# Kernel tuning notes

Measured on AMD Instinct MI355X. Metric: run time of the kernel, lower is better.

Reference implementation:

```python
import jax, jax.numpy as jnp
import numpy as np

N_EMBD = 2048
N_HEAD = 32
HEAD_SIZE = 64          # n_embd // n_head
MIX_DIM = 64            # RWKV-6 time-mix LoRA dim
DECAY_DIM = 128         # RWKV-6 decay LoRA dim
BATCH = 1024
STATE_ROWS = (2 + HEAD_SIZE) * 1  # single block, i = 0


def setup_inputs() -> dict:
    key = jax.random.key(0)
    ks = jax.random.split(key, 32)
    rn = lambda k, shp, s=0.02: jax.random.normal(k, shp, jnp.float32) * s
    d = {}
    d['x'] = jax.random.normal(ks[0], (BATCH, N_EMBD), jnp.float32)
    d['state'] = jax.random.normal(ks[1], (BATCH, STATE_ROWS, N_EMBD), jnp.float32) * 0.1
    d['ln1_w'] = jnp.ones((N_EMBD,), jnp.float32)
    d['ln1_b'] = jnp.zeros((N_EMBD,), jnp.float32)
    d['ln2_w'] = jnp.ones((N_EMBD,), jnp.float32)
    d['ln2_b'] = jnp.zeros((N_EMBD,), jnp.float32)
    d['maa_x'] = rn(ks[2], (N_EMBD,), 0.1)
    d['maa_w'] = rn(ks[3], (N_EMBD,), 0.1)
    d['maa_k'] = rn(ks[4], (N_EMBD,), 0.1)
    d['maa_v'] = rn(ks[5], (N_EMBD,), 0.1)
    d['maa_r'] = rn(ks[6], (N_EMBD,), 0.1)
    d['maa_g'] = rn(ks[7], (N_EMBD,), 0.1)
    d['maa_w1'] = rn(ks[8], (N_EMBD, 5 * MIX_DIM))
    d['maa_w2'] = rn(ks[9], (5, MIX_DIM, N_EMBD))
    d['decay'] = rn(ks[10], (N_EMBD,), 0.5) - 4.0  # typical negative log-decay
    d['decay_w1'] = rn(ks[11], (N_EMBD, DECAY_DIM))
    d['decay_w2'] = rn(ks[12], (DECAY_DIM, N_EMBD))
    d['faaaa'] = rn(ks[13], (N_HEAD, HEAD_SIZE, 1), 0.1)
    d['Wr'] = rn(ks[14], (N_EMBD, N_EMBD))
    d['Wk'] = rn(ks[15], (N_EMBD, N_EMBD))
    d['Wv'] = rn(ks[16], (N_EMBD, N_EMBD))
    d['Wo'] = rn(ks[17], (N_EMBD, N_EMBD))
    d['Wg'] = rn(ks[18], (N_EMBD, N_EMBD))
    d['gn_w'] = jnp.ones((N_EMBD,), jnp.float32)
    d['gn_b'] = jnp.zeros((N_EMBD,), jnp.float32)
    d['ffn_maa_k'] = rn(ks[19], (N_EMBD,), 0.1)
    d['ffn_maa_r'] = rn(ks[20], (N_EMBD,), 0.1)
    d['ffn_Wk'] = rn(ks[21], (N_EMBD, N_EMBD))
    d['ffn_Wr'] = rn(ks[22], (N_EMBD, N_EMBD))
    d['ffn_Wv'] = rn(ks[23], (N_EMBD, N_EMBD))
    d['i'] = 0
    return d


def _ln(x, w, b):
    mu = jnp.mean(x, -1, keepdims=True)
    var = jnp.var(x, -1, keepdims=True)
    return (x - mu) * jax.lax.rsqrt(var + 1e-5) * w + b


def reference(x, state, ln1_w, ln1_b, ln2_w, ln2_b,
              maa_x, maa_w, maa_k, maa_v, maa_r, maa_g, maa_w1, maa_w2,
              decay, decay_w1, decay_w2, faaaa,
              Wr, Wk, Wv, Wo, Wg, gn_w, gn_b,
              ffn_maa_k, ffn_maa_r, ffn_Wk, ffn_Wr, ffn_Wv, i):
    B = x.shape[0]
    H, S = N_HEAD, HEAD_SIZE
    # ---------------- time mixing ----------------
    xn = _ln(x, ln1_w, ln1_b)
    i1 = (2 + S) * i + 1
    sx = state[:, i1] - xn                                  # token shift delta
    xxx = xn + sx * maa_x
    xxx = jnp.tanh(xxx @ maa_w1).reshape(B, 5, 1, MIX_DIM)
    xxx = jnp.matmul(xxx, maa_w2).reshape(B, 5, N_EMBD)     # [B,5,E]
    mw, mk, mv, mr, mg = (xxx[:, j] for j in range(5))
    xw = xn + sx * (maa_w + mw)
    xk = xn + sx * (maa_k + mk)
    xv = xn + sx * (maa_v + mv)
    xr = xn + sx * (maa_r + mr)
    xg = xn + sx * (maa_g + mg)
    w = decay + jnp.tanh(xw @ decay_w1) @ decay_w2          # [B,E]
    w = jnp.exp(-jnp.exp(w.reshape(B, H, S, 1)))            # decay gate
    r = (xr @ Wr.T).reshape(B, H, 1, S)
    k = (xk @ Wk.T).reshape(B, H, S, 1)
    v = (xv @ Wv.T).reshape(B, H, 1, S)
    g = jax.nn.silu(xg @ Wg.T)
    s = state[:, (2 + S) * i + 2:(2 + S) * (i + 1), :].reshape(B, H, S, S)
    a = jnp.matmul(k, v)                                    # [B,H,S,S] outer product
    y = jnp.matmul(r, faaaa * a + s).reshape(B, N_EMBD)     # wkv readout
    # group norm (n_head groups over n_embd channels)
    yg = y.reshape(B, H, S)
    mu = jnp.mean(yg, -1, keepdims=True)
    var = jnp.var(yg, -1, keepdims=True)
    yg = ((yg - mu) * jax.lax.rsqrt(var + 1e-5)).reshape(B, N_EMBD) * gn_w + gn_b
    x1 = x + (yg * g) @ Wo.T
    # ---------------- channel mixing ----------------
    xn2 = _ln(x1, ln2_w, ln2_b)
    i0 = (2 + S) * i
    sx2 = state[:, i0] - xn2
    xk2 = xn2 + sx2 * ffn_maa_k
    xr2 = xn2 + sx2 * ffn_maa_r
    rr = jax.nn.sigmoid(xr2 @ ffn_Wr.T)
    kk = jnp.square(jax.nn.relu(xk2 @ ffn_Wk.T))
    return x1 + rr * (kk @ ffn_Wv.T)
```

## Files before the change

kernel.cpp:

```cpp
#include <hip/hip_runtime.h>
#include <cstdint>
#include <cstddef>

typedef unsigned short u16;
typedef __attribute__((ext_vector_type(8))) short bf16x8;
typedef __attribute__((ext_vector_type(4))) float f32x4;

#define DEV __device__ __forceinline__

DEV u16 f2bf(float f) {
  uint32_t b = __float_as_uint(f);
  b += 0x7fffu + ((b >> 16) & 1u);
  return (u16)(b >> 16);
}
DEV float bf2f(u16 u) { return __uint_as_float(((uint32_t)u) << 16); }

DEV void gl16(const u16* g, u16* l) {
  __builtin_amdgcn_global_load_lds(
      (const __attribute__((address_space(1))) void*)g,
      (__attribute__((address_space(3))) void*)l, 16, 0, 0);
}

struct CvtArgs { const float* s[8]; };

__global__ __launch_bounds__(256) void k_cvt(CvtArgs a,
                                             const float* __restrict__ w1,
                                             const float* __restrict__ w2,
                                             u16* __restrict__ dst,
                                             u16* __restrict__ w1t,
                                             u16* __restrict__ w2t) {
  if (blockIdx.x < 16384) {
    size_t idx = ((size_t)blockIdx.x * 256 + threadIdx.x) * 8;
    int w = (int)(idx >> 22);
    size_t off = idx & ((1u << 22) - 1);
    const float* s = a.s[w];
    float4 v0 = *(const float4*)(s + off);
    float4 v1 = *(const float4*)(s + off + 4);
    uint4 p; u16* pl = (u16*)&p;
    pl[0] = f2bf(v0.x); pl[1] = f2bf(v0.y); pl[2] = f2bf(v0.z); pl[3] = f2bf(v0.w);
    pl[4] = f2bf(v1.x); pl[5] = f2bf(v1.y); pl[6] = f2bf(v1.z); pl[7] = f2bf(v1.w);
    *(uint4*)(dst + ((size_t)w << 22) + off) = p;
  } else {
    int idx = (blockIdx.x - 16384) * 256 + threadIdx.x;
    if (idx < 655360) {
      int n = idx >> 11, k = idx & 2047;
      w1t[idx] = f2bf(w1[(size_t)k * 320 + n]);
    } else {
      int r = idx - 655360;
      int j = r >> 17, q = r & 131071;
      int n = q >> 6, k2 = q & 63;
      w2t[r] = f2bf(w2[((size_t)(j + 1) * 64 + k2) * 2048 + n]);
    }
  }
}

__global__ __launch_bounds__(256) void k_tanhpack(const float* __restrict__ p2,
                                                  u16* __restrict__ xb) {
  int idx = blockIdx.x * 256 + threadIdx.x;
  float s = p2[idx] + p2[327680 + idx] + p2[2 * 327680 + idx] + p2[3 * 327680 + idx];
  xb[idx] = f2bf(tanhf(s));
}

__global__ __launch_bounds__(256) void k_act(const u16* __restrict__ p8,
                                             u16* __restrict__ rr, u16* __restrict__ kk) {
  const size_t S = 2097152;
  int gid = blockIdx.x * 256 + threadIdx.x;
  size_t e0 = (size_t)(gid & 262143) * 8;
  int isk = gid >= 262144;
  const u16* base = p8 + (isk ? 4 * S : 0) + e0;
  float acc[8] = {};
#pragma unroll
  for (int s = 0; s < 4; ++s) {
    uint4 v = *(const uint4*)(base + (size_t)s * S);
    u16* vl = (u16*)&v;
#pragma unroll
    for (int j = 0; j < 8; ++j) acc[j] += bf2f(vl[j]);
  }
  uint4 p; u16* pl = (u16*)&p;
  if (!isk) {
#pragma unroll
    for (int j = 0; j < 8; ++j) pl[j] = f2bf(1.f / (1.f + __expf(-acc[j])));
    *(uint4*)(rr + e0) = p;
  } else {
#pragma unroll
    for (int j = 0; j < 8; ++j) { float r = acc[j] > 0.f ? acc[j] : 0.f; pl[j] = f2bf(r * r); }
    *(uint4*)(kk + e0) = p;
  }
}

__global__ __launch_bounds__(256) void k_fin(const float* __restrict__ x1,
                                             const u16* __restrict__ p9,
                                             const u16* __restrict__ rr,
                                             float* __restrict__ out) {
  const size_t S = 2097152;
  size_t e0 = ((size_t)blockIdx.x * 256 + threadIdx.x) * 8;
  float acc[8] = {};
#pragma unroll
  for (int s = 0; s < 4; ++s) {
    uint4 v = *(const uint4*)(p9 + (size_t)s * S + e0);
    u16* vl = (u16*)&v;
#pragma unroll
    for (int j = 0; j < 8; ++j) acc[j] += bf2f(vl[j]);
  }
  float4 x0 = *(const float4*)(x1 + e0), x4 = *(const float4*)(x1 + e0 + 4);
  float xv[8] = {x0.x, x0.y, x0.z, x0.w, x4.x, x4.y, x4.z, x4.w};
  uint4 rv = *(const uint4*)(rr + e0); u16* rl = (u16*)&rv;
  float o[8];
#pragma unroll
  for (int j = 0; j < 8; ++j) o[j] = xv[j] + bf2f(rl[j]) * acc[j];
  *(float4*)(out + e0) = make_float4(o[0], o[1], o[2], o[3]);
  *(float4*)(out + e0 + 4) = make_float4(o[4], o[5], o[6], o[7]);
}

__global__ __launch_bounds__(256) void k_ln_mix1(
    const float* __restrict__ x, const float* __restrict__ state,
    const int* __restrict__ ip,
    const float* __restrict__ lw, const float* __restrict__ lb,
    const float* __restrict__ mx,
    u16* __restrict__ xn_o, u16* __restrict__ sx_o, u16* __restrict__ a1_o) {
  int b = blockIdx.x, t = threadIdx.x;
  const float* xr = x + (size_t)b * 2048;
  float4 v0 = *(const float4*)(xr + t * 8);
  float4 v1 = *(const float4*)(xr + t * 8 + 4);
  float xv[8] = {v0.x, v0.y, v0.z, v0.w, v1.x, v1.y, v1.z, v1.w};
  float s1 = 0.f, s2 = 0.f;
#pragma unroll
  for (int j = 0; j < 8; ++j) { s1 += xv[j]; s2 += xv[j] * xv[j]; }
#pragma unroll
  for (int off = 32; off; off >>= 1) { s1 += __shfl_xor(s1, off); s2 += __shfl_xor(s2, off); }
  __shared__ float ls1[4], ls2[4];
  int w = t >> 6;
  if ((t & 63) == 0) { ls1[w] = s1; ls2[w] = s2; }
  __syncthreads();
  s1 = ls1[0] + ls1[1] + ls1[2] + ls1[3];
  s2 = ls2[0] + ls2[1] + ls2[2] + ls2[3];
  float mu = s1 * (1.0f / 2048.0f);
  float var = s2 * (1.0f / 2048.0f) - mu * mu;
  float rs = rsqrtf(var + 1e-5f);
  const float* st = state + ((size_t)b * 66 + (size_t)66 * ip[0] + 1) * 2048;
  int e0 = t * 8;
  uint4 xnp, sxp, a1p;
  u16* xnl = (u16*)&xnp; u16* sxl = (u16*)&sxp; u16* a1l = (u16*)&a1p;
#pragma unroll
  for (int j = 0; j < 8; ++j) {
    int e = e0 + j;
    float xn = (xv[j] - mu) * rs * lw[e] + lb[e];
    float sxv = st[e] - xn;
    xnl[j] = f2bf(xn); sxl[j] = f2bf(sxv); a1l[j] = f2bf(xn + sxv * mx[e]);
  }
  size_t o = (size_t)b * 2048 + e0;
  *(uint4*)(xn_o + o) = xnp;
  *(uint4*)(sx_o + o) = sxp;
  *(uint4*)(a1_o + o) = a1p;
}

__global__ __launch_bounds__(256) void k_ln_mix2(
    const float* __restrict__ x, const u16* __restrict__ p6,
    const float* __restrict__ state, const int* __restrict__ ip,
    const float* __restrict__ lw, const float* __restrict__ lb,
    const float* __restrict__ mk, const float* __restrict__ mr,
    u16* __restrict__ xk_o, u16* __restrict__ xr_o, float* __restrict__ x1_o) {
  const size_t S = 2097152;
  int b = blockIdx.x, t = threadIdx.x;
  size_t off = (size_t)b * 2048 + t * 8;
  float4 v0 = *(const float4*)(x + off);
  float4 v1 = *(const float4*)(x + off + 4);
  float xv[8] = {v0.x, v0.y, v0.z, v0.w, v1.x, v1.y, v1.z, v1.w};
#pragma unroll
  for (int s = 0; s < 4; ++s) {
    uint4 v = *(const uint4*)(p6 + (size_t)s * S + off);
    u16* vl = (u16*)&v;
#pragma unroll
    for (int j = 0; j < 8; ++j) xv[j] += bf2f(vl[j]);
  }
  *(float4*)(x1_o + off) = make_float4(xv[0], xv[1], xv[2], xv[3]);
  *(float4*)(x1_o + off + 4) = make_float4(xv[4], xv[5], xv[6], xv[7]);
  float s1 = 0.f, s2 = 0.f;
#pragma unroll
  for (int j = 0; j < 8; ++j) { s1 += xv[j]; s2 += xv[j] * xv[j]; }
#pragma unroll
  for (int off2 = 32; off2; off2 >>= 1) { s1 += __shfl_xor(s1, off2); s2 += __shfl_xor(s2, off2); }
  __shared__ float ls1[4], ls2[4];
  int w = t >> 6;
  if ((t & 63) == 0) { ls1[w] = s1; ls2[w] = s2; }
  __syncthreads();
  s1 = ls1[0] + ls1[1] + ls1[2] + ls1[3];
  s2 = ls2[0] + ls2[1] + ls2[2] + ls2[3];
  float mu = s1 * (1.0f / 2048.0f);
  float var = s2 * (1.0f / 2048.0f) - mu * mu;
  float rs = rsqrtf(var + 1e-5f);
  const float* st = state + ((size_t)b * 66 + (size_t)66 * ip[0] + 0) * 2048;
  int e0 = t * 8;
  uint4 xkp, xrp;
  u16* xkl = (u16*)&xkp; u16* xrl = (u16*)&xrp;
#pragma unroll
  for (int j = 0; j < 8; ++j) {
    int e = e0 + j;
    float xn = (xv[j] - mu) * rs * lw[e] + lb[e];
    float sxv = st[e] - xn;
    xkl[j] = f2bf(xn + sxv * mk[e]);
    xrl[j] = f2bf(xn + sxv * mr[e]);
  }
  *(uint4*)(xk_o + off) = xkp;
  *(uint4*)(xr_o + off) = xrp;
}

enum { EP_STORE = 0, EP_SILU, EP_MIX, EP_STOREF };

struct GemmDesc {
  const u16* A; const u16* B; void* C;
  const void* p1; const void* p2; const float* pvec;
  int lda, ldb, ldc, N, K, k0, ep;
};
struct GemmBatch { GemmDesc g[8]; int bpg; };

__global__ __launch_bounds__(256, 3) void k_gemm(GemmBatch bat) {
  int gi = blockIdx.x / bat.bpg;
  int bid = blockIdx.x % bat.bpg;
  GemmDesc g = bat.g[gi];
  int ntn = (g.N + 127) >> 7;
  int m0 = (bid / ntn) << 7;
  int n0 = (bid % ntn) << 7;
  __shared__ u16 As[2][128 * 32];
  __shared__ u16 Bs[2][128 * 32];
  int t = threadIdx.x, w = t >> 6, lane = t & 63;
  int wm = w >> 1, wn = w & 1;
  int lr = lane & 15, kb = (lane >> 4) * 8;
  const u16* Ab = g.A + (size_t)(m0 + w * 32 + (lane >> 2)) * g.lda + (lane & 3) * 8;
  const u16* Bb = g.B + (size_t)(n0 + w * 32 + (lane >> 2)) * g.ldb + (lane & 3) * 8;
  int a16 = 16 * g.lda, b16 = 16 * g.ldb;
  int aoff = (w * 32) * 32;
  f32x4 acc[4][4] = {};
  int nt = g.K >> 5;

  auto stage = [&](int buf, int kk) {
    u16* Ad = (u16*)As + buf * 4096 + aoff;
    u16* Bd = (u16*)Bs + buf * 4096 + aoff;
    gl16(Ab + kk, Ad);
    gl16(Ab + kk + a16, Ad + 512);
    gl16(Bb + kk, Bd);
    gl16(Bb + kk + b16, Bd + 512);
  };

  stage(0, g.k0);
  __syncthreads();
  int cur = 0;
  for (int ti = 0; ti < nt; ++ti) {
    if (ti + 1 < nt) stage(cur ^ 1, g.k0 + (ti + 1) * 32);
    const u16* Ac = (const u16*)As + cur * 4096;
// ... 11 lines not shown
      for (int n = 0; n < 4; ++n)
        acc[m][n] = __builtin_amdgcn_mfma_f32_16x16x32_bf16(af[m], bfr[n], acc[m][n], 0, 0, 0);
    __syncthreads();
    cur ^= 1;
  }

  int ep = g.ep;
#pragma unroll
  for (int m = 0; m < 4; ++m) {
    int grow0 = m0 + wm * 64 + m * 16 + (lane >> 4) * 4;
#pragma unroll
    for (int n = 0; n < 4; ++n) {
      int gc = n0 + wn * 64 + n * 16 + lr;
      if (gc >= g.N) continue;
#pragma unroll
      for (int q = 0; q < 4; ++q) {
        size_t ci = (size_t)(grow0 + q) * g.ldc + gc;
        float v = acc[m][n][q];
        switch (ep) {
          case EP_STORE: ((u16*)g.C)[ci] = f2bf(v); break;
          case EP_MIX: {
            float xn = bf2f(((const u16*)g.p1)[ci]);
            float sxv = bf2f(((const u16*)g.p2)[ci]);
            ((u16*)g.C)[ci] = f2bf(xn + sxv * (g.pvec[gc] + v));
          } break;
          case EP_STOREF: ((float*)g.C)[ci] = v; break;
          default: break;
        }
      }
    }
  }
}

__global__ __launch_bounds__(512, 2) void k_gemm2(GemmBatch bat) {
  extern __shared__ u16 lds[];
  int nwg = gridDim.x;
  int wg0 = blockIdx.x;
  int wg = (wg0 & 7) * (nwg >> 3) + (wg0 >> 3);
  int gi = wg / bat.bpg;
  int bid = wg % bat.bpg;
  GemmDesc g = bat.g[gi];
  int ntn = (g.N + 255) >> 8;
  int m0 = (bid / ntn) << 7;
  int n0 = (bid % ntn) << 8;
  int t = threadIdx.x, wv = t >> 6, lane = t & 63;
  int wm = wv >> 2, wn = wv & 3;
  int lr = lane & 15, hi = lane >> 4;

  const u16* asrc[2]; const u16* bsrc[4];
#pragma unroll
  for (int j = 0; j < 2; ++j) {
    int cid = t + 512 * j, r = cid >> 3, c = cid & 7;
    asrc[j] = g.A + (size_t)(m0 + r) * g.lda + ((c ^ (r & 7)) << 3);
  }
#pragma unroll
  for (int j = 0; j < 4; ++j) {
    int cid = t + 512 * j, r = cid >> 3, c = cid & 7;
    bsrc[j] = g.B + (size_t)(n0 + r) * g.ldb + ((c ^ (r & 7)) << 3);
  }
  int au = wv * 512;

  auto stage = [&](int buf, int k) {
    u16* base = lds + buf * 24576;
#pragma unroll
    for (int j = 0; j < 2; ++j) gl16(asrc[j] + k, base + au + j * 4096);
#pragma unroll
    for (int j = 0; j < 4; ++j) gl16(bsrc[j] + k, base + 8192 + au + j * 4096);
  };

  int arow[4], brow[4];
#pragma unroll
  for (int m = 0; m < 4; ++m) arow[m] = wm * 64 + m * 16 + lr;
#pragma unroll
  for (int n = 0; n < 4; ++n) brow[n] = wn * 64 + n * 16 + lr;

  f32x4 acc[4][4] = {};
  int nt = g.K >> 6;
  stage(0, g.k0);
  if (nt > 1) stage(1, g.k0 + 64);

  for (int ti = 0; ti < nt; ++ti) {
    if (ti + 1 < nt) asm volatile("s_waitcnt vmcnt(6)" ::: "memory");
    else             asm volatile("s_waitcnt vmcnt(0)" ::: "memory");
    __builtin_amdgcn_sched_barrier(0);
    __builtin_amdgcn_s_barrier();
    __builtin_amdgcn_sched_barrier(0);
    const u16* buf = lds + (ti % 3) * 24576;
    bf16x8 af[4][2], bf[4][2];
#pragma unroll
    for (int m = 0; m < 4; ++m)
#pragma unroll
      for (int ks = 0; ks < 2; ++ks)
        af[m][ks] = *(const bf16x8*)(buf + arow[m] * 64 + ((((ks << 2) + hi) ^ (arow[m] & 7)) << 3));
#pragma unroll
    for (int n = 0; n < 4; ++n)
#pragma unroll
      for (int ks = 0; ks < 2; ++ks)
        bf[n][ks] = *(const bf16x8*)(buf + 8192 + brow[n] * 64 + ((((ks << 2) + hi) ^ (brow[n] & 7)) << 3));
    if (ti + 2 < nt) stage((ti + 2) % 3, g.k0 + (ti + 2) * 64);
    __builtin_amdgcn_s_setprio(1);
#pragma unroll
    for (int m = 0; m < 4; ++m)
#pragma unroll
      for (int n = 0; n < 4; ++n)
#pragma unroll
        for (int ks = 0; ks < 2; ++ks)
          acc[m][n] = __builtin_amdgcn_mfma_f32_16x16x32_bf16(af[m][ks], bf[n][ks], acc[m][n], 0, 0, 0);
    __builtin_amdgcn_s_setprio(0);
  }

  int ep = g.ep;
#pragma unroll
  for (int m = 0; m < 4; ++m) {
    int grow0 = m0 + wm * 64 + m * 16 + hi * 4;
#pragma unroll
    for (int n = 0; n < 4; ++n) {
      int gc = n0 + wn * 64 + n * 16 + lr;
#pragma unroll
      for (int q = 0; q < 4; ++q) {
        size_t ci = (size_t)(grow0 + q) * g.ldc + gc;
        float v = acc[m][n][q];
        switch (ep) {
          case EP_STORE: ((u16*)g.C)[ci] = f2bf(v); break;
          case EP_SILU:  ((u16*)g.C)[ci] = f2bf(v / (1.f + __expf(-v))); break;
          case EP_STOREF: ((float*)g.C)[ci] = v; break;
          default: break;
        }
      }
    }
  }
}

__global__ __launch_bounds__(512, 2) void k_gemm3(GemmBatch bat) {
  extern __shared__ u16 lds[];
  int nwg = gridDim.x;
  int wg0 = blockIdx.x;
  int wg = (wg0 & 7) * (nwg >> 3) + (wg0 >> 3);
  GemmDesc g = bat.g[wg / bat.bpg];
  int bid = wg % bat.bpg;
  int ntn = g.N >> 8;
  int m0 = (bid / ntn) << 8;
  int n0 = (bid % ntn) << 8;
  int t = threadIdx.x, wv = t >> 6, lane = t & 63;
  int wm = wv >> 2, wn = wv & 3;
  int lr = lane & 15, hi = lane >> 4;

  const u16* asrc[4]; const u16* bsrc[4];
#pragma unroll
  for (int j = 0; j < 4; ++j) {
    int cid = t + 512 * j, r = cid >> 3, c = cid & 7;
    asrc[j] = g.A + (size_t)(m0 + r) * g.lda + ((c ^ (r & 7)) << 3);
    bsrc[j] = g.B + (size_t)(n0 + r) * g.ldb + ((c ^ (r & 7)) << 3);
  }
  int au = wv * 512;

  auto stage = [&](int buf, int k) {
    u16* ab = lds + buf * 32768 + au;
    u16* bb = lds + buf * 32768 + 16384 + au;
#pragma unroll
    for (int j = 0; j < 4; ++j) gl16(asrc[j] + k, ab + j * 4096);
#pragma unroll
    for (int j = 0; j < 4; ++j) gl16(bsrc[j] + k, bb + j * 4096);
  };

  int arow[8], brow[4];
#pragma unroll
  for (int m = 0; m < 8; ++m) arow[m] = wm * 128 + m * 16 + lr;
#pragma unroll
  for (int n = 0; n < 4; ++n) brow[n] = wn * 64 + n * 16 + lr;

  f32x4 acc[8][4] = {};
  int nt = g.K >> 6;
  stage(0, g.k0);
  if (nt > 1) stage(1, g.k0 + 64);

  for (int ti = 0; ti < nt; ++ti) {
    if (ti + 1 < nt) asm volatile("s_waitcnt vmcnt(8)" ::: "memory");
    else             asm volatile("s_waitcnt vmcnt(0)" ::: "memory");
    __builtin_amdgcn_sched_barrier(0);
    __builtin_amdgcn_s_barrier();
    __builtin_amdgcn_sched_barrier(0);
    const u16* buf = lds + (ti & 1) * 32768;
#pragma unroll
    for (int ks = 0; ks < 2; ++ks) {
      bf16x8 af[8], bf[4];
#pragma unroll
      for (int m = 0; m < 8; ++m)
        af[m] = *(const bf16x8*)(buf + arow[m] * 64 + ((((ks << 2) + hi) ^ (arow[m] & 7)) << 3));
#pragma unroll
      for (int n = 0; n < 4; ++n)
        bf[n] = *(const bf16x8*)(buf + 16384 + brow[n] * 64 + ((((ks << 2) + hi) ^ (brow[n] & 7)) << 3));
      __builtin_amdgcn_s_setprio(1);
#pragma unroll
      for (int m = 0; m < 8; ++m)
#pragma unroll
        for (int n = 0; n < 4; ++n)
          acc[m][n] = __builtin_amdgcn_mfma_f32_16x16x32_bf16(af[m], bf[n], acc[m][n], 0, 0, 0);
      __builtin_amdgcn_s_setprio(0);
    }
    __builtin_amdgcn_sched_barrier(0);
    __builtin_amdgcn_s_barrier();
    __builtin_amdgcn_sched_barrier(0);
    if (ti + 2 < nt) stage(ti & 1, g.k0 + (ti + 2) * 64);
  }

#pragma unroll
  for (int m = 0; m < 8; ++m) {
    int grow0 = m0 + wm * 128 + m * 16 + hi * 4;
#pragma unroll
    for (int n = 0; n < 4; ++n) {
      int gc = n0 + wn * 64 + n * 16 + lr;
#pragma unroll
      for (int q = 0; q < 4; ++q)
        ((u16*)g.C)[(size_t)(grow0 + q) * g.ldc + gc] = f2bf(acc[m][n][q]);
    }
  }
}

__global__ __launch_bounds__(256) void k_wkv(
    const u16* __restrict__ p4,
    const float* __restrict__ state, const int* __restrict__ ip,
    const float* __restrict__ fa, const float* __restrict__ gw,
    const float* __restrict__ gbias, u16* __restrict__ t_o) {
  const size_t S = 2097152;
  int t = threadIdx.x, w = t >> 6, lane = t & 63;
  int flat = blockIdx.x * 4 + w;
  int b = flat >> 5, h = flat & 31;
  size_t base = ((size_t)b << 11) + (h << 6) + lane;
  float r  = bf2f(p4[base])         + bf2f(p4[S + base]);
  float kv = bf2f(p4[2 * S + base]) + bf2f(p4[3 * S + base]);
  float vv = bf2f(p4[4 * S + base]) + bf2f(p4[5 * S + base]);
  float gs = bf2f(p4[6 * S + base]) + bf2f(p4[7 * S + base]);
  float gg = gs / (1.f + __expf(-gs));
  float f  = fa[(h << 6) + lane];
  __shared__ float rs[4][64];
  rs[w][lane] = r;
  __syncthreads();
  float c = r * f * kv;
#pragma unroll
  for (int off = 32; off; off >>= 1) c += __shfl_xor(c, off);

  const float* sp = state + ((size_t)b * 66 + (size_t)66 * ip[0] + 2 + 2 * h) * 2048;
  int q = lane >> 4, jj = lane & 15;
  float yp0 = 0.f, yp1 = 0.f, yp2 = 0.f, yp3 = 0.f;
#pragma unroll
  for (int ib = 0; ib < 16; ++ib) {
    int i = ib * 4 + q;
// ... 40 lines not shown
  const float* faaaa  = (const float*)d_in[17];
  const float* Wr     = (const float*)d_in[18];
  const float* Wk     = (const float*)d_in[19];
  const float* Wv     = (const float*)d_in[20];
  const float* Wo     = (const float*)d_in[21];
  const float* Wg     = (const float*)d_in[22];
  const float* gn_w   = (const float*)d_in[23];
  const float* gn_b   = (const float*)d_in[24];
  const float* fmk    = (const float*)d_in[25];
  const float* fmr    = (const float*)d_in[26];
  const float* fWk    = (const float*)d_in[27];
  const float* fWr    = (const float*)d_in[28];
  const float* fWv    = (const float*)d_in[29];
  const int*   ip     = (const int*)d_in[30];
  float* out = (float*)d_out;

  char* wsb = (char*)d_ws;
  const size_t MB = 1ull << 20;
  u16* wbf   = (u16*)(wsb + 0 * MB);
  u16* w1t   = (u16*)(wsb + 64 * MB);
  u16* w2t   = (u16*)(wsb + 66 * MB);
  u16* xn    = (u16*)(wsb + 68 * MB);
  u16* sx    = (u16*)(wsb + 72 * MB);
  u16* a1    = (u16*)(wsb + 76 * MB);
  float* p2  = (float*)(wsb + 80 * MB);
  u16* xxx   = (u16*)(wsb + 86 * MB);
  u16* xk    = (u16*)(wsb + 87 * MB);
  u16* xv    = (u16*)(wsb + 91 * MB);
  u16* xr    = (u16*)(wsb + 95 * MB);
  u16* xg    = (u16*)(wsb + 99 * MB);
  u16* p4    = (u16*)(wsb + 103 * MB);
  u16* tb    = (u16*)(wsb + 135 * MB);
  u16* p6    = (u16*)(wsb + 139 * MB);
  float* x1  = (float*)(wsb + 155 * MB);
  u16* xk2   = (u16*)(wsb + 163 * MB);
  u16* xr2   = (u16*)(wsb + 167 * MB);
  u16* p8    = (u16*)(wsb + 171 * MB);
  u16* rr    = (u16*)(wsb + 203 * MB);
  u16* kkb   = (u16*)(wsb + 207 * MB);
  u16* p9    = (u16*)(wsb + 211 * MB);

  const size_t WSQ = 4194304, S = 2097152;
  u16* bWr = wbf + 0 * WSQ; u16* bWk = wbf + 1 * WSQ; u16* bWv = wbf + 2 * WSQ;
  u16* bWg = wbf + 3 * WSQ; u16* bWo = wbf + 4 * WSQ; u16* bfWr = wbf + 5 * WSQ;
  u16* bfWk = wbf + 6 * WSQ; u16* bfWv = wbf + 7 * WSQ;

  auto mkd = [](const u16* A, const u16* B, void* C, const void* p1,
                const void* p2_, const float* pvec, int lda, int ldb, int ldc,
                int N, int K, int k0, int epf) {
    GemmDesc d; d.A = A; d.B = B; d.C = C; d.p1 = p1; d.p2 = p2_; d.pvec = pvec;
    d.lda = lda; d.ldb = ldb; d.ldc = ldc; d.N = N; d.K = K; d.k0 = k0; d.ep = epf;
    return d;
  };

  static const int LDS2 = 147456;
  static const int LDS3 = 131072;
  hipFuncSetAttribute((const void*)k_gemm2,
                      hipFuncAttributeMaxDynamicSharedMemorySize, LDS2);
  hipFuncSetAttribute((const void*)k_gemm3,
                      hipFuncAttributeMaxDynamicSharedMemorySize, LDS3);

  {
    CvtArgs ca; ca.s[0] = Wr; ca.s[1] = Wk; ca.s[2] = Wv; ca.s[3] = Wg;
    ca.s[4] = Wo; ca.s[5] = fWr; ca.s[6] = fWk; ca.s[7] = fWv;
    k_cvt<<<20992, 256, 0, stream>>>(ca, maa_w1, maa_w2, wbf, w1t, w2t);
  }

  k_ln_mix1<<<1024, 256, 0, stream>>>(x, state, ip, ln1_w, ln1_b, maa_x, xn, sx, a1);

  {
    GemmBatch g{}; g.bpg = 8 * 3;
    for (int j = 0; j < 4; ++j)
      g.g[j] = mkd(a1, w1t, p2 + (size_t)j * 327680, nullptr, nullptr, nullptr,
                   2048, 2048, 320, 320, 512, j * 512, EP_STOREF);
    k_gemm<<<96, 256, 0, stream>>>(g);
  }
  k_tanhpack<<<1280, 256, 0, stream>>>(p2, xxx);

  {
    GemmBatch g{}; g.bpg = 8 * 16;
    const float* mv[4] = {maa_k, maa_v, maa_r, maa_g};
    u16* tv[4] = {xk, xv, xr, xg};
    for (int j = 1; j <= 4; ++j)
      g.g[j - 1] = mkd(xxx + j * 64, w2t + (size_t)(j - 1) * 131072, tv[j - 1],
                       xn, sx, mv[j - 1], 320, 64, 2048, 2048, 64, 0, EP_MIX);
    k_gemm<<<512, 256, 0, stream>>>(g);
  }

  {
    GemmBatch g{}; g.bpg = 32;
    const u16* av[4] = {xr, xk, xv, xg};
    const u16* bv[4] = {bWr, bWk, bWv, bWg};
    for (int q = 0; q < 4; ++q)
      for (int s = 0; s < 2; ++s)
        g.g[q * 2 + s] = mkd(av[q], bv[q], p4 + (size_t)(q * 2 + s) * S,
                             nullptr, nullptr, nullptr, 2048, 2048, 2048,
                             2048, 1024, s * 1024, EP_STORE);
    k_gemm3<<<256, 512, LDS3, stream>>>(g);
  }

  k_wkv<<<8192, 256, 0, stream>>>(p4, state, ip, faaaa, gn_w, gn_b, tb);

  {
    GemmBatch g{}; g.bpg = 8 * 8;
    for (int s = 0; s < 4; ++s)
      g.g[s] = mkd(tb, bWo, p6 + (size_t)s * S, nullptr, nullptr, nullptr,
                   2048, 2048, 2048, 2048, 512, s * 512, EP_STORE);
    k_gemm2<<<256, 512, LDS2, stream>>>(g);
  }

  k_ln_mix2<<<1024, 256, 0, stream>>>(x, p6, state, ip, ln2_w, ln2_b, fmk, fmr,
                                      xk2, xr2, x1);

  {
    GemmBatch g{}; g.bpg = 32;
    for (int s = 0; s < 4; ++s) {
      g.g[s]     = mkd(xr2, bfWr, p8 + (size_t)s * S, nullptr, nullptr, nullptr,
                       2048, 2048, 2048, 2048, 512, s * 512, EP_STORE);
      g.g[4 + s] = mkd(xk2, bfWk, p8 + (size_t)(4 + s) * S, nullptr, nullptr, nullptr,
                       2048, 2048, 2048, 2048, 512, s * 512, EP_STORE);
    }
    k_gemm3<<<256, 512, LDS3, stream>>>(g);
  }
  k_act<<<2048, 256, 0, stream>>>(p8, rr, kkb);

  {
    GemmBatch g{}; g.bpg = 8 * 8;
    for (int s = 0; s < 4; ++s)
      g.g[s] = mkd(kkb, bfWv, p9 + (size_t)s * S, nullptr, nullptr, nullptr,
                   2048, 2048, 2048, 2048, 512, s * 512, EP_STORE);
    k_gemm2<<<256, 512, LDS2, stream>>>(g);
  }

  k_fin<<<1024, 256, 0, stream>>>(x1, p9, rr, out);
}
```

Measured before the change: 326.3 us.

## Rework gemm3 with 4-stage k32 pipeline, drop gemm2, fuse LN1 into convert

New measurement: 349.2 us. +7.0%, slower.

```diff
diff --git a/kernel.cpp b/kernel.cpp
--- a/kernel.cpp
+++ b/kernel.cpp
@@ -23,12 +23,15 @@
 
 struct CvtArgs { const float* s[8]; };
 
-__global__ __launch_bounds__(256) void k_cvt(CvtArgs a,
-                                             const float* __restrict__ w1,
-                                             const float* __restrict__ w2,
-                                             u16* __restrict__ dst,
-                                             u16* __restrict__ w1t,
-                                             u16* __restrict__ w2t) {
+__global__ __launch_bounds__(256) void k_cvt_ln(
+    CvtArgs a, const float* __restrict__ w1, const float* __restrict__ w2,
+    u16* __restrict__ dst, u16* __restrict__ w1t, u16* __restrict__ w2t,
+    const float* __restrict__ x, const float* __restrict__ state,
+    const int* __restrict__ ip,
+    const float* __restrict__ lw, const float* __restrict__ lb,
+    const float* __restrict__ mx,
+    u16* __restrict__ xn_o, u16* __restrict__ sx_o, u16* __restrict__ a1_o) {
+  __shared__ float ls1[4], ls2[4];
   if (blockIdx.x < 16384) {
     size_t idx = ((size_t)blockIdx.x * 256 + threadIdx.x) * 8;
     int w = (int)(idx >> 22);
@@ -40,7 +43,7 @@
     pl[0] = f2bf(v0.x); pl[1] = f2bf(v0.y); pl[2] = f2bf(v0.z); pl[3] = f2bf(v0.w);
     pl[4] = f2bf(v1.x); pl[5] = f2bf(v1.y); pl[6] = f2bf(v1.z); pl[7] = f2bf(v1.w);
     *(uint4*)(dst + ((size_t)w << 22) + off) = p;
-  } else {
+  } else if (blockIdx.x < 20992) {
     int idx = (blockIdx.x - 16384) * 256 + threadIdx.x;
     if (idx < 655360) {
       int n = idx >> 11, k = idx & 2047;
@@ -51,6 +54,40 @@
       int n = q >> 6, k2 = q & 63;
       w2t[r] = f2bf(w2[((size_t)(j + 1) * 64 + k2) * 2048 + n]);
     }
+  } else {
+    int b = blockIdx.x - 20992, t = threadIdx.x;
+    const float* xr = x + (size_t)b * 2048;
+    float4 v0 = *(const float4*)(xr + t * 8);
+    float4 v1 = *(const float4*)(xr + t * 8 + 4);
+    float xv[8] = {v0.x, v0.y, v0.z, v0.w, v1.x, v1.y, v1.z, v1.w};
+    float s1 = 0.f, s2 = 0.f;
+#pragma unroll
+    for (int j = 0; j < 8; ++j) { s1 += xv[j]; s2 += xv[j] * xv[j]; }
+#pragma unroll
+    for (int off = 32; off; off >>= 1) { s1 += __shfl_xor(s1, off); s2 += __shfl_xor(s2, off); }
+    int w = t >> 6;
+    if ((t & 63) == 0) { ls1[w] = s1; ls2[w] = s2; }
+    __syncthreads();
+    s1 = ls1[0] + ls1[1] + ls1[2] + ls1[3];
+    s2 = ls2[0] + ls2[1] + ls2[2] + ls2[3];
+    float mu = s1 * (1.0f / 2048.0f);
+    float var = s2 * (1.0f / 2048.0f) - mu * mu;
+    float rs = rsqrtf(var + 1e-5f);
+    const float* st = state + ((size_t)b * 66 + (size_t)66 * ip[0] + 1) * 2048;
+    int e0 = t * 8;
+    uint4 xnp, sxp, a1p;
+    u16* xnl = (u16*)&xnp; u16* sxl = (u16*)&sxp; u16* a1l = (u16*)&a1p;
+#pragma unroll
+    for (int j = 0; j < 8; ++j) {
+      int e = e0 + j;
+      float xn = (xv[j] - mu) * rs * lw[e] + lb[e];
+      float sxv = st[e] - xn;
+      xnl[j] = f2bf(xn); sxl[j] = f2bf(sxv); a1l[j] = f2bf(xn + sxv * mx[e]);
+    }
+    size_t o = (size_t)b * 2048 + e0;
+    *(uint4*)(xn_o + o) = xnp;
+    *(uint4*)(sx_o + o) = sxp;
+    *(uint4*)(a1_o + o) = a1p;
   }
 }
 
@@ -96,7 +133,7 @@
   size_t e0 = ((size_t)blockIdx.x * 256 + threadIdx.x) * 8;
   float acc[8] = {};
 #pragma unroll
-  for (int s = 0; s < 4; ++s) {
+  for (int s = 0; s < 8; ++s) {
     uint4 v = *(const uint4*)(p9 + (size_t)s * S + e0);
     u16* vl = (u16*)&v;
 #pragma unroll
@@ -110,48 +147,6 @@
   for (int j = 0; j < 8; ++j) o[j] = xv[j] + bf2f(rl[j]) * acc[j];
   *(float4*)(out + e0) = make_float4(o[0], o[1], o[2], o[3]);
   *(float4*)(out + e0 + 4) = make_float4(o[4], o[5], o[6], o[7]);
-}
-
-__global__ __launch_bounds__(256) void k_ln_mix1(
-    const float* __restrict__ x, const float* __restrict__ state,
-    const int* __restrict__ ip,
-    const float* __restrict__ lw, const float* __restrict__ lb,
-    const float* __restrict__ mx,
-    u16* __restrict__ xn_o, u16* __restrict__ sx_o, u16* __restrict__ a1_o) {
-  int b = blockIdx.x, t = threadIdx.x;
-  const float* xr = x + (size_t)b * 2048;
-  float4 v0 = *(const float4*)(xr + t * 8);
-  float4 v1 = *(const float4*)(xr + t * 8 + 4);
-  float xv[8] = {v0.x, v0.y, v0.z, v0.w, v1.x, v1.y, v1.z, v1.w};
-  float s1 = 0.f, s2 = 0.f;
-#pragma unroll
-  for (int j = 0; j < 8; ++j) { s1 += xv[j]; s2 += xv[j] * xv[j]; }
-#pragma unroll
-  for (int off = 32; off; off >>= 1) { s1 += __shfl_xor(s1, off); s2 += __shfl_xor(s2, off); }
-  __shared__ float ls1[4], ls2[4];
-  int w = t >> 6;
-  if ((t & 63) == 0) { ls1[w] = s1; ls2[w] = s2; }
-  __syncthreads();
-  s1 = ls1[0] + ls1[1] + ls1[2] + ls1[3];
-  s2 = ls2[0] + ls2[1] + ls2[2] + ls2[3];
-  float mu = s1 * (1.0f / 2048.0f);
-  float var = s2 * (1.0f / 2048.0f) - mu * mu;
-  float rs = rsqrtf(var + 1e-5f);
-  const float* st = state + ((size_t)b * 66 + (size_t)66 * ip[0] + 1) * 2048;
-  int e0 = t * 8;
-  uint4 xnp, sxp, a1p;
-  u16* xnl = (u16*)&xnp; u16* sxl = (u16*)&sxp; u16* a1l = (u16*)&a1p;
-#pragma unroll
-  for (int j = 0; j < 8; ++j) {
-    int e = e0 + j;
-    float xn = (xv[j] - mu) * rs * lw[e] + lb[e];
-    float sxv = st[e] - xn;
-    xnl[j] = f2bf(xn); sxl[j] = f2bf(sxv); a1l[j] = f2bf(xn + sxv * mx[e]);
-  }
-  size_t o = (size_t)b * 2048 + e0;
-  *(uint4*)(xn_o + o) = xnp;
-  *(uint4*)(sx_o + o) = sxp;
-  *(uint4*)(a1_o + o) = a1p;
 }
 
 __global__ __launch_bounds__(256) void k_ln_mix2(
@@ -167,7 +162,7 @@
   float4 v1 = *(const float4*)(x + off + 4);
   float xv[8] = {v0.x, v0.y, v0.z, v0.w, v1.x, v1.y, v1.z, v1.w};
 #pragma unroll
-  for (int s = 0; s < 4; ++s) {
+  for (int s = 0; s < 8; ++s) {
     uint4 v = *(const uint4*)(p6 + (size_t)s * S + off);
     u16* vl = (u16*)&v;
 #pragma unroll
@@ -292,105 +287,6 @@
   }
 }
 
-__global__ __launch_bounds__(512, 2) void k_gemm2(GemmBatch bat) {
-  extern __shared__ u16 lds[];
-  int nwg = gridDim.x;
-  int wg0 = blockIdx.x;
-  int wg = (wg0 & 7) * (nwg >> 3) + (wg0 >> 3);
-  int gi = wg / bat.bpg;
-  int bid = wg % bat.bpg;
-  GemmDesc g = bat.g[gi];
-  int ntn = (g.N + 255) >> 8;
-  int m0 = (bid / ntn) << 7;
-  int n0 = (bid % ntn) << 8;
-  int t = threadIdx.x, wv = t >> 6, lane = t & 63;
-  int wm = wv >> 2, wn = wv & 3;
-  int lr = lane & 15, hi = lane >> 4;
-
-  const u16* asrc[2]; const u16* bsrc[4];
-#pragma unroll
-  for (int j = 0; j < 2; ++j) {
-    int cid = t + 512 * j, r = cid >> 3, c = cid & 7;
-    asrc[j] = g.A + (size_t)(m0 + r) * g.lda + ((c ^ (r & 7)) << 3);
-  }
-#pragma unroll
-  for (int j = 0; j < 4; ++j) {
-    int cid = t + 512 * j, r = cid >> 3, c = cid & 7;
-    bsrc[j] = g.B + (size_t)(n0 + r) * g.ldb + ((c ^ (r & 7)) << 3);
-  }
-  int au = wv * 512;
-
-  auto stage = [&](int buf, int k) {
-    u16* base = lds + buf * 24576;
-#pragma unroll
-    for (int j = 0; j < 2; ++j) gl16(asrc[j] + k, base + au + j * 4096);
-#pragma unroll
-    for (int j = 0; j < 4; ++j) gl16(bsrc[j] + k, base + 8192 + au + j * 4096);
-  };
-
-  int arow[4], brow[4];
-#pragma unroll
-  for (int m = 0; m < 4; ++m) arow[m] = wm * 64 + m * 16 + lr;
-#pragma unroll
-  for (int n = 0; n < 4; ++n) brow[n] = wn * 64 + n * 16 + lr;
-
-  f32x4 acc[4][4] = {};
-  int nt = g.K >> 6;
-  stage(0, g.k0);
-  if (nt > 1) stage(1, g.k0 + 64);
-
-  for (int ti = 0; ti < nt; ++ti) {
-    if (ti + 1 < nt) asm volatile("s_waitcnt vmcnt(6)" ::: "memory");
-    else             asm volatile("s_waitcnt vmcnt(0)" ::: "memory");
-    __builtin_amdgcn_sched_barrier(0);
-    __builtin_amdgcn_s_barrier();
-    __builtin_amdgcn_sched_barrier(0);
-    const u16* buf = lds + (ti % 3) * 24576;
-    bf16x8 af[4][2], bf[4][2];
-#pragma unroll
-    for (int m = 0; m < 4; ++m)
-#pragma unroll
-      for (int ks = 0; ks < 2; ++ks)
-        af[m][ks] = *(const bf16x8*)(buf + arow[m] * 64 + ((((ks << 2) + hi) ^ (arow[m] & 7)) << 3));
-#pragma unroll
-    for (int n = 0; n < 4; ++n)
-#pragma unroll
-      for (int ks = 0; ks < 2; ++ks)
-        bf[n][ks] = *(const bf16x8*)(buf + 8192 + brow[n] * 64 + ((((ks << 2) + hi) ^ (brow[n] & 7)) << 3));
-    if (ti + 2 < nt) stage((ti + 2) % 3, g.k0 + (ti + 2) * 64);
-    __builtin_amdgcn_s_setprio(1);
-#pragma unroll
-    for (int m = 0; m < 4; ++m)
-#pragma unroll
-      for (int n = 0; n < 4; ++n)
-#pragma unroll
-        for (int ks = 0; ks < 2; ++ks)
-          acc[m][n] = __builtin_amdgcn_mfma_f32_16x16x32_bf16(af[m][ks], bf[n][ks], acc[m][n], 0, 0, 0);
-    __builtin_amdgcn_s_setprio(0);
-  }
-
-  int ep = g.ep;
-#pragma unroll
-  for (int m = 0; m < 4; ++m) {
-    int grow0 = m0 + wm * 64 + m * 16 + hi * 4;
-#pragma unroll
-    for (int n = 0; n < 4; ++n) {
-      int gc = n0 + wn * 64 + n * 16 + lr;
-#pragma unroll
-      for (int q = 0; q < 4; ++q) {
-        size_t ci = (size_t)(grow0 + q) * g.ldc + gc;
-        float v = acc[m][n][q];
-        switch (ep) {
-          case EP_STORE: ((u16*)g.C)[ci] = f2bf(v); break;
-          case EP_SILU:  ((u16*)g.C)[ci] = f2bf(v / (1.f + __expf(-v))); break;
-          case EP_STOREF: ((float*)g.C)[ci] = v; break;
-          default: break;
-        }
-      }
-    }
-  }
-}
-
 __global__ __launch_bounds__(512, 2) void k_gemm3(GemmBatch bat) {
   extern __shared__ u16 lds[];
   int nwg = gridDim.x;
@@ -405,65 +301,85 @@
   int wm = wv >> 2, wn = wv & 3;
   int lr = lane & 15, hi = lane >> 4;
 
-  const u16* asrc[4]; const u16* bsrc[4];
-#pragma unroll
-  for (int j = 0; j < 4; ++j) {
-    int cid = t + 512 * j, r = cid >> 3, c = cid & 7;
-    asrc[j] = g.A + (size_t)(m0 + r) * g.lda + ((c ^ (r & 7)) << 3);
-    bsrc[j] = g.B + (size_t)(n0 + r) * g.ldb + ((c ^ (r & 7)) << 3);
-  }
+  int r = t >> 2;
+  int cc = (((t & 3) ^ (r & 3)) << 3);
+  const u16* sa0 = g.A + (size_t)(m0 + r) * g.lda + cc;
+  const u16* sa1 = g.A + (size_t)(m0 + 128 + r) * g.lda + cc;
+  const u16* sb0 = g.B + (size_t)(n0 + r) * g.ldb + cc;
+  const u16* sb1 = g.B + (size_t)(n0 + 128 + r) * g.ldb + cc;
   int au = wv * 512;
-
-  auto stage = [&](int buf, int k) {
-    u16* ab = lds + buf * 32768 + au;
-    u16* bb = lds + buf * 32768 + 16384 + au;
-#pragma unroll
-    for (int j = 0; j < 4; ++j) gl16(asrc[j] + k, ab + j * 4096);
-#pragma unroll
-    for (int j = 0; j < 4; ++j) gl16(bsrc[j] + k, bb + j * 4096);
-  };
-
-  int arow[8], brow[4];
-#pragma unroll
-  for (int m = 0; m < 8; ++m) arow[m] = wm * 128 + m * 16 + lr;
-#pragma unroll
-  for (int n = 0; n < 4; ++n) brow[n] = wn * 64 + n * 16 + lr;
+  u16* dummy = lds + 65536 + au;
+
+  int aswz = (hi ^ (lr & 3)) << 3;
+  int abase = wm * 4096 + lr * 32 + aswz;
+  int bbase = 8192 + (wv & 2) * 2048 + (wv & 1) * 2048 + lr * 32 + aswz;
+
+  int nt = g.K >> 5;
+  {
+    int k0e = g.k0;
+    gl16(sa0 + k0e, lds + au);            gl16(sb0 + k0e, lds + 8192 + au);
+    gl16(sa1 + k0e, lds + 4096 + au);     gl16(sb1 + k0e, lds + 12288 + au);
+    int k1e = g.k0 + 32;
+    gl16(sa0 + k1e, lds + 16384 + au);    gl16(sb0 + k1e, lds + 16384 + 8192 + au);
+    gl16(sa1 + k1e, lds + 16384 + 4096 + au); gl16(sb1 + k1e, lds + 16384 + 12288 + au);
+  }
+  asm volatile("s_waitcnt vmcnt(4)" ::: "memory");
+  __builtin_amdgcn_sched_barrier(0);
+  __builtin_amdgcn_s_barrier();
+  __builtin_amdgcn_sched_barrier(0);
 
   f32x4 acc[8][4] = {};
-  int nt = g.K >> 6;
-  stage(0, g.k0);
-  if (nt > 1) stage(1, g.k0 + 64);
-
-  for (int ti = 0; ti < nt; ++ti) {
-    if (ti + 1 < nt) asm volatile("s_waitcnt vmcnt(8)" ::: "memory");
-    else             asm volatile("s_waitcnt vmcnt(0)" ::: "memory");
+  for (int kt = 0; kt < nt; ++kt) {
+    const u16* bp = lds + (kt & 3) * 16384;
+    int real = (kt + 2 < nt);
+    int tgt = real ? kt + 2 : nt - 1;
+    int ko = g.k0 + tgt * 32;
+    u16* db = real ? lds + ((kt + 2) & 3) * 16384 : (u16*)0;
+
+    gl16(sa0 + ko, real ? db + au : dummy);
+    gl16(sb0 + ko, real ? db + 8192 + au : dummy);
+    bf16x8 a0_[8], bA[2];
+#pragma unroll
+    for (int m = 0; m < 8; ++m) a0_[m] = *(const bf16x8*)(bp + abase + m * 512);
+    bA[0] = *(const bf16x8*)(bp + bbase);
+    bA[1] = *(const bf16x8*)(bp + bbase + 512);
+    asm volatile("s_waitcnt vmcnt(4)" ::: "memory");
     __builtin_amdgcn_sched_barrier(0);
     __builtin_amdgcn_s_barrier();
     __builtin_amdgcn_sched_barrier(0);
-    const u16* buf = lds + (ti & 1) * 32768;
-#pragma unroll
-    for (int ks = 0; ks < 2; ++ks) {
-      bf16x8 af[8], bf[4];
-#pragma unroll
-      for (int m = 0; m < 8; ++m)
-        af[m] = *(const bf16x8*)(buf + arow[m] * 64 + ((((ks << 2) + hi) ^ (arow[m] & 7)) << 3));
-#pragma unroll
-      for (int n = 0; n < 4; ++n)
-        bf[n] = *(const bf16x8*)(buf + 16384 + brow[n] * 64 + ((((ks << 2) + hi) ^ (brow[n] & 7)) << 3));
-      __builtin_amdgcn_s_setprio(1);
-#pragma unroll
-      for (int m = 0; m < 8; ++m)
-#pragma unroll
-        for (int n = 0; n < 4; ++n)
-          acc[m][n] = __builtin_amdgcn_mfma_f32_16x16x32_bf16(af[m], bf[n], acc[m][n], 0, 0, 0);
-      __builtin_amdgcn_s_setprio(0);
-    }
+    __builtin_amdgcn_s_setprio(1);
+#pragma unroll
+    for (int m = 0; m < 8; ++m) {
+      acc[m][0] = __builtin_amdgcn_mfma_f32_16x16x32_bf16(a0_[m], bA[0], acc[m][0], 0, 0, 0);
+      acc[m][1] = __builtin_amdgcn_mfma_f32_16x16x32_bf16(a0_[m], bA[1], acc[m][1], 0, 0, 0);
+    }
+    __builtin_amdgcn_s_setprio(0);
     __builtin_amdgcn_sched_barrier(0);
     __builtin_amdgcn_s_barrier();
     __builtin_amdgcn_sched_barrier(0);
-    if (ti + 2 < nt) stage(ti & 1, g.k0 + (ti + 2) * 64);
-  }
-
+
+    gl16(sa1 + ko, real ? db + 4096 + au : dummy);
+    gl16(sb1 + ko, real ? db + 12288 + au : dummy);
+    bf16x8 bB[2];
+    bB[0] = *(const bf16x8*)(bp + bbase + 1024);
+    bB[1] = *(const bf16x8*)(bp + bbase + 1536);
+    asm volatile("s_waitcnt vmcnt(4)" ::: "memory");
+    __builtin_amdgcn_sched_barrier(0);
+    __builtin_amdgcn_s_barrier();
+    __builtin_amdgcn_sched_barrier(0);
+    __builtin_amdgcn_s_setprio(1);
+#pragma unroll
+    for (int m = 0; m < 8; ++m) {
+      acc[m][2] = __builtin_amdgcn_mfma_f32_16x16x32_bf16(a0_[m], bB[0], acc[m][2], 0, 0, 0);
+      acc[m][3] = __builtin_amdgcn_mfma_f32_16x16x32_bf16(a0_[m], bB[1], acc[m][3], 0, 0, 0);
+    }
+    __builtin_amdgcn_s_setprio(0);
+    __builtin_amdgcn_sched_barrier(0);
+    __builtin_amdgcn_s_barrier();
+    __builtin_amdgcn_sched_barrier(0);
+  }
+
+  int ep = g.ep;
 #pragma unroll
   for (int m = 0; m < 8; ++m) {
     int grow0 = m0 + wm * 128 + m * 16 + hi * 4;
@@ -471,8 +387,12 @@
     for (int n = 0; n < 4; ++n) {
       int gc = n0 + wn * 64 + n * 16 + lr;
 #pragma unroll
-      for (int q = 0; q < 4; ++q)
-        ((u16*)g.C)[(size_t)(grow0 + q) * g.ldc + gc] = f2bf(acc[m][n][q]);
+      for (int q = 0; q < 4; ++q) {
+        size_t ci = (size_t)(grow0 + q) * g.ldc + gc;
+        float v = acc[m][n][q];
+        if (ep == EP_STOREF) ((float*)g.C)[ci] = v;
+        else                 ((u16*)g.C)[ci] = f2bf(v);
+      }
     }
   }
 }
@@ -579,13 +499,13 @@
   u16* p4    = (u16*)(wsb + 103 * MB);
   u16* tb    = (u16*)(wsb + 135 * MB);
   u16* p6    = (u16*)(wsb + 139 * MB);
-  float* x1  = (float*)(wsb + 155 * MB);
-  u16* xk2   = (u16*)(wsb + 163 * MB);
-  u16* xr2   = (u16*)(wsb + 167 * MB);
-  u16* p8    = (u16*)(wsb + 171 * MB);
-  u16* rr    = (u16*)(wsb + 203 * MB);
-  u16* kkb   = (u16*)(wsb + 207 * MB);
-  u16* p9    = (u16*)(wsb + 211 * MB);
+  float* x1  = (float*)(wsb + 171 * MB);
+  u16* xk2   = (u16*)(wsb + 179 * MB);
+  u16* xr2   = (u16*)(wsb + 183 * MB);
+  u16* p8    = (u16*)(wsb + 187 * MB);
+  u16* rr    = (u16*)(wsb + 219 * MB);
+  u16* kkb   = (u16*)(wsb + 223 * MB);
+  u16* p9    = (u16*)(wsb + 227 * MB);
 
   const size_t WSQ = 4194304, S = 2097152;
   u16* bWr = wbf + 0 * WSQ; u16* bWk = wbf + 1 * WSQ; u16* bWv = wbf + 2 * WSQ;
@@ -600,20 +520,16 @@
     return d;
   };
 
-  static const int LDS2 = 147456;
-  static const int LDS3 = 131072;
-  hipFuncSetAttribute((const void*)k_gemm2,
-                      hipFuncAttributeMaxDynamicSharedMemorySize, LDS2);
+  static const int LDS3 = 139264;
   hipFuncSetAttribute((const void*)k_gemm3,
                       hipFuncAttributeMaxDynamicSharedMemorySize, LDS3);
 
   {
     CvtArgs ca; ca.s[0] = Wr; ca.s[1] = Wk; ca.s[2] = Wv; ca.s[3] = Wg;
     ca.s[4] = Wo; ca.s[5] = fWr; ca.s[6] = fWk; ca.s[7] = fWv;
-    k_cvt<<<20992, 256, 0, stream>>>(ca, maa_w1, maa_w2, wbf, w1t, w2t);
-  }
-
-  k_ln_mix1<<<1024, 256, 0, stream>>>(x, state, ip, ln1_w, ln1_b, maa_x, xn, sx, a1);
+    k_cvt_ln<<<22016, 256, 0, stream>>>(ca, maa_w1, maa_w2, wbf, w1t, w2t,
+                                        x, state, ip, ln1_w, ln1_b, maa_x, xn, sx, a1);
+  }
 
   {
     GemmBatch g{}; g.bpg = 8 * 3;
@@ -649,11 +565,11 @@
   k_wkv<<<8192, 256, 0, stream>>>(p4, state, ip, faaaa, gn_w, gn_b, tb);
 
   {
-    GemmBatch g{}; g.bpg = 8 * 8;
-    for (int s = 0; s < 4; ++s)
+    GemmBatch g{}; g.bpg = 32;
+    for (int s = 0; s < 8; ++s)
       g.g[s] = mkd(tb, bWo, p6 + (size_t)s * S, nullptr, nullptr, nullptr,
-                   2048, 2048, 2048, 2048, 512, s * 512, EP_STORE);
-    k_gemm2<<<256, 512, LDS2, stream>>>(g);
+                   2048, 2048, 2048, 2048, 256, s * 256, EP_STORE);
+    k_gemm3<<<256, 512, LDS3, stream>>>(g);
   }
 
   k_ln_mix2<<<1024, 256, 0, stream>>>(x, p6, state, ip, ln2_w, ln2_b, fmk, fmr,
@@ -672,11 +588,11 @@
   k_act<<<2048, 256, 0, stream>>>(p8, rr, kkb);
 
   {
-    GemmBatch g{}; g.bpg = 8 * 8;
-    for (int s = 0; s < 4; ++s)
+    GemmBatch g{}; g.bpg = 32;
+    for (int s = 0; s < 8; ++s)
       g.g[s] = mkd(kkb, bfWv, p9 + (size_t)s * S, nullptr, nullptr, nullptr,
-                   2048, 2048, 2048, 2048, 512, s * 512, EP_STORE);
-    k_gemm2<<<256, 512, LDS2, stream>>>(g);
+                   2048, 2048, 2048, 2048, 256, s * 256, EP_STORE);
+    k_gemm3<<<256, 512, LDS3, stream>>>(g);
   }
 
   k_fin<<<1024, 256, 0, stream>>>(x1, p9, rr, out);
```

## Overlap big weight bf16 conversion with small LoRA GEMMs and fuse LN into cvt

Applied to the files above, without the earlier changes.

Measured after the change: 320.2 us. Within noise of the previous version (-1.9%).

```diff
diff --git a/kernel.cpp b/kernel.cpp
--- a/kernel.cpp
+++ b/kernel.cpp
@@ -23,25 +23,17 @@
 
 struct CvtArgs { const float* s[8]; };
 
-__global__ __launch_bounds__(256) void k_cvt(CvtArgs a,
-                                             const float* __restrict__ w1,
-                                             const float* __restrict__ w2,
-                                             u16* __restrict__ dst,
-                                             u16* __restrict__ w1t,
-                                             u16* __restrict__ w2t) {
-  if (blockIdx.x < 16384) {
-    size_t idx = ((size_t)blockIdx.x * 256 + threadIdx.x) * 8;
-    int w = (int)(idx >> 22);
-    size_t off = idx & ((1u << 22) - 1);
-    const float* s = a.s[w];
-    float4 v0 = *(const float4*)(s + off);
-    float4 v1 = *(const float4*)(s + off + 4);
-    uint4 p; u16* pl = (u16*)&p;
-    pl[0] = f2bf(v0.x); pl[1] = f2bf(v0.y); pl[2] = f2bf(v0.z); pl[3] = f2bf(v0.w);
-    pl[4] = f2bf(v1.x); pl[5] = f2bf(v1.y); pl[6] = f2bf(v1.z); pl[7] = f2bf(v1.w);
-    *(uint4*)(dst + ((size_t)w << 22) + off) = p;
-  } else {
-    int idx = (blockIdx.x - 16384) * 256 + threadIdx.x;
+__global__ __launch_bounds__(256) void k_cvt_ln(
+    const float* __restrict__ w1, const float* __restrict__ w2,
+    u16* __restrict__ w1t, u16* __restrict__ w2t,
+    const float* __restrict__ x, const float* __restrict__ state,
+    const int* __restrict__ ip,
+    const float* __restrict__ lw, const float* __restrict__ lb,
+    const float* __restrict__ mx,
+    u16* __restrict__ xn_o, u16* __restrict__ sx_o, u16* __restrict__ a1_o) {
+  __shared__ float ls1[4], ls2[4];
+  if (blockIdx.x < 4608) {
+    int idx = blockIdx.x * 256 + threadIdx.x;
     if (idx < 655360) {
       int n = idx >> 11, k = idx & 2047;
       w1t[idx] = f2bf(w1[(size_t)k * 320 + n]);
@@ -51,6 +43,40 @@
       int n = q >> 6, k2 = q & 63;
       w2t[r] = f2bf(w2[((size_t)(j + 1) * 64 + k2) * 2048 + n]);
     }
+  } else {
+    int b = blockIdx.x - 4608, t = threadIdx.x;
+    const float* xr = x + (size_t)b * 2048;
+    float4 v0 = *(const float4*)(xr + t * 8);
+    float4 v1 = *(const float4*)(xr + t * 8 + 4);
+    float xv[8] = {v0.x, v0.y, v0.z, v0.w, v1.x, v1.y, v1.z, v1.w};
+    float s1 = 0.f, s2 = 0.f;
+#pragma unroll
+    for (int j = 0; j < 8; ++j) { s1 += xv[j]; s2 += xv[j] * xv[j]; }
+#pragma unroll
+    for (int off = 32; off; off >>= 1) { s1 += __shfl_xor(s1, off); s2 += __shfl_xor(s2, off); }
+    int w = t >> 6;
+    if ((t & 63) == 0) { ls1[w] = s1; ls2[w] = s2; }
+    __syncthreads();
+    s1 = ls1[0] + ls1[1] + ls1[2] + ls1[3];
+    s2 = ls2[0] + ls2[1] + ls2[2] + ls2[3];
+    float mu = s1 * (1.0f / 2048.0f);
+    float var = s2 * (1.0f / 2048.0f) - mu * mu;
+    float rs = rsqrtf(var + 1e-5f);
+    const float* st = state + ((size_t)b * 66 + (size_t)66 * ip[0] + 1) * 2048;
+    int e0 = t * 8;
+    uint4 xnp, sxp, a1p;
+    u16* xnl = (u16*)&xnp; u16* sxl = (u16*)&sxp; u16* a1l = (u16*)&a1p;
+#pragma unroll
+    for (int j = 0; j < 8; ++j) {
+      int e = e0 + j;
+      float xn = (xv[j] - mu) * rs * lw[e] + lb[e];
+      float sxv = st[e] - xn;
+      xnl[j] = f2bf(xn); sxl[j] = f2bf(sxv); a1l[j] = f2bf(xn + sxv * mx[e]);
+    }
+    size_t o = (size_t)b * 2048 + e0;
+    *(uint4*)(xn_o + o) = xnp;
+    *(uint4*)(sx_o + o) = sxp;
+    *(uint4*)(a1_o + o) = a1p;
   }
 }
 
@@ -110,48 +136,6 @@
   for (int j = 0; j < 8; ++j) o[j] = xv[j] + bf2f(rl[j]) * acc[j];
   *(float4*)(out + e0) = make_float4(o[0], o[1], o[2], o[3]);
   *(float4*)(out + e0 + 4) = make_float4(o[4], o[5], o[6], o[7]);
-}
-
-__global__ __launch_bounds__(256) void k_ln_mix1(
-    const float* __restrict__ x, const float* __restrict__ state,
-    const int* __restrict__ ip,
-    const float* __restrict__ lw, const float* __restrict__ lb,
-    const float* __restrict__ mx,
-    u16* __restrict__ xn_o, u16* __restrict__ sx_o, u16* __restrict__ a1_o) {
-  int b = blockIdx.x, t = threadIdx.x;
-  const float* xr = x + (size_t)b * 2048;
-  float4 v0 = *(const float4*)(xr + t * 8);
-  float4 v1 = *(const float4*)(xr + t * 8 + 4);
-  float xv[8] = {v0.x, v0.y, v0.z, v0.w, v1.x, v1.y, v1.z, v1.w};
-  float s1 = 0.f, s2 = 0.f;
-#pragma unroll
-  for (int j = 0; j < 8; ++j) { s1 += xv[j]; s2 += xv[j] * xv[j]; }
-#pragma unroll
-  for (int off = 32; off; off >>= 1) { s1 += __shfl_xor(s1, off); s2 += __shfl_xor(s2, off); }
-  __shared__ float ls1[4], ls2[4];
-  int w = t >> 6;
-  if ((t & 63) == 0) { ls1[w] = s1; ls2[w] = s2; }
-  __syncthreads();
-  s1 = ls1[0] + ls1[1] + ls1[2] + ls1[3];
-  s2 = ls2[0] + ls2[1] + ls2[2] + ls2[3];
-  float mu = s1 * (1.0f / 2048.0f);
-  float var = s2 * (1.0f / 2048.0f) - mu * mu;
-  float rs = rsqrtf(var + 1e-5f);
-  const float* st = state + ((size_t)b * 66 + (size_t)66 * ip[0] + 1) * 2048;
-  int e0 = t * 8;
-  uint4 xnp, sxp, a1p;
-  u16* xnl = (u16*)&xnp; u16* sxl = (u16*)&sxp; u16* a1l = (u16*)&a1p;
-#pragma unroll
-  for (int j = 0; j < 8; ++j) {
-    int e = e0 + j;
-    float xn = (xv[j] - mu) * rs * lw[e] + lb[e];
-    float sxv = st[e] - xn;
-    xnl[j] = f2bf(xn); sxl[j] = f2bf(sxv); a1l[j] = f2bf(xn + sxv * mx[e]);
-  }
-  size_t o = (size_t)b * 2048 + e0;
-  *(uint4*)(xn_o + o) = xnp;
-  *(uint4*)(sx_o + o) = sxp;
-  *(uint4*)(a1_o + o) = a1p;
 }
 
 __global__ __launch_bounds__(256) void k_ln_mix2(
@@ -214,7 +198,22 @@
 };
 struct GemmBatch { GemmDesc g[8]; int bpg; };
 
-__global__ __launch_bounds__(256, 3) void k_gemm(GemmBatch bat) {
+__global__ __launch_bounds__(256, 3) void k_gemmc(GemmBatch bat, int ngemm,
+                                                  CvtArgs ca, u16* __restrict__ cdst,
+                                                  int cvtoff) {
+  if (blockIdx.x >= ngemm) {
+    size_t idx = ((size_t)(blockIdx.x - ngemm + cvtoff) * 256 + threadIdx.x) * 8;
+    int w = (int)(idx >> 22);
+    size_t off = idx & ((1u << 22) - 1);
+    const float* s = ca.s[w];
+    float4 v0 = *(const float4*)(s + off);
+    float4 v1 = *(const float4*)(s + off + 4);
+    uint4 p; u16* pl = (u16*)&p;
+    pl[0] = f2bf(v0.x); pl[1] = f2bf(v0.y); pl[2] = f2bf(v0.z); pl[3] = f2bf(v0.w);
+    pl[4] = f2bf(v1.x); pl[5] = f2bf(v1.y); pl[6] = f2bf(v1.z); pl[7] = f2bf(v1.w);
+    *(uint4*)(cdst + ((size_t)w << 22) + off) = p;
+    return;
+  }
   int gi = blockIdx.x / bat.bpg;
   int bid = blockIdx.x % bat.bpg;
   GemmDesc g = bat.g[gi];
@@ -600,6 +599,9 @@
     return d;
   };
 
+  CvtArgs ca; ca.s[0] = Wr; ca.s[1] = Wk; ca.s[2] = Wv; ca.s[3] = Wg;
+  ca.s[4] = Wo; ca.s[5] = fWr; ca.s[6] = fWk; ca.s[7] = fWv;
+
   static const int LDS2 = 147456;
   static const int LDS3 = 131072;
   hipFuncSetAttribute((const void*)k_gemm2,
@@ -607,20 +609,15 @@
   hipFuncSetAttribute((const void*)k_gemm3,
                       hipFuncAttributeMaxDynamicSharedMemorySize, LDS3);
 
-  {
-    CvtArgs ca; ca.s[0] = Wr; ca.s[1] = Wk; ca.s[2] = Wv; ca.s[3] = Wg;
-    ca.s[4] = Wo; ca.s[5] = fWr; ca.s[6] = fWk; ca.s[7] = fWv;
-    k_cvt<<<20992, 256, 0, stream>>>(ca, maa_w1, maa_w2, wbf, w1t, w2t);
-  }
-
-  k_ln_mix1<<<1024, 256, 0, stream>>>(x, state, ip, ln1_w, ln1_b, maa_x, xn, sx, a1);
+  k_cvt_ln<<<5632, 256, 0, stream>>>(maa_w1, maa_w2, w1t, w2t,
+                                     x, state, ip, ln1_w, ln1_b, maa_x, xn, sx, a1);
 
   {
     GemmBatch g{}; g.bpg = 8 * 3;
     for (int j = 0; j < 4; ++j)
       g.g[j] = mkd(a1, w1t, p2 + (size_t)j * 327680, nullptr, nullptr, nullptr,
                    2048, 2048, 320, 320, 512, j * 512, EP_STOREF);
-    k_gemm<<<96, 256, 0, stream>>>(g);
+    k_gemmc<<<96 + 8192, 256, 0, stream>>>(g, 96, ca, wbf, 0);
   }
   k_tanhpack<<<1280, 256, 0, stream>>>(p2, xxx);
 
@@ -631,7 +628,7 @@
     for (int j = 1; j <= 4; ++j)
       g.g[j - 1] = mkd(xxx + j * 64, w2t + (size_t)(j - 1) * 131072, tv[j - 1],
                        xn, sx, mv[j - 1], 320, 64, 2048, 2048, 64, 0, EP_MIX);
-    k_gemm<<<512, 256, 0, stream>>>(g);
+    k_gemmc<<<512 + 8192, 256, 0, stream>>>(g, 512, ca, wbf, 8192);
   }
 
   {
```
